# Optimization experiments

Hardware: AMD Instinct MI355X
Metric: run time of the kernel (lower is better)

Reference implementation:

```python
import jax, jax.numpy as jnp
import numpy as np
from jax.ops import segment_sum

N_NODES = 50000
N_EDGES = 800000
D_IN, D_HID, D_OUT = 128, 128, 64


def setup_inputs() -> dict:
    key = jax.random.key(0)
    ks = jax.random.split(key, 7)
    return {
        "src": jax.random.randint(ks[0], (N_EDGES,), 0, N_NODES, dtype=jnp.int32),
        "dst": jax.random.randint(ks[1], (N_EDGES,), 0, N_NODES, dtype=jnp.int32),
        "x": jax.random.normal(ks[2], (N_NODES, D_IN), dtype=jnp.float32),
        "W1": jax.random.normal(ks[3], (D_IN, D_HID), dtype=jnp.float32) * (1.0 / np.sqrt(D_IN)),
        "b1": jnp.zeros((D_HID,), dtype=jnp.float32),
        "W2": jax.random.normal(ks[4], (D_HID, D_OUT), dtype=jnp.float32) * (1.0 / np.sqrt(D_HID)),
        "b2": jnp.zeros((D_OUT,), dtype=jnp.float32),
    }


def _gcn_layer(src, dst, x, W, b, inv_sqrt_out, inv_sqrt_in):
    # DGL GraphConv, norm='both': h = D_in^{-1/2} A D_out^{-1/2} (x W) + b
    h = (x * inv_sqrt_out[:, None]) @ W          # transform first (in >= out)
    msg = h[src]                                  # gather source messages [E, d]
    agg = segment_sum(msg, dst, num_segments=x.shape[0])
    return agg * inv_sqrt_in[:, None] + b


def reference(src, dst, x, W1, b1, W2, b2):
    n = x.shape[0]
    ones = jnp.ones((src.shape[0],), dtype=x.dtype)
    deg_out = jnp.clip(segment_sum(ones, src, num_segments=n), 1.0)
    deg_in = jnp.clip(segment_sum(ones, dst, num_segments=n), 1.0)
    inv_sqrt_out = jax.lax.rsqrt(deg_out)
    inv_sqrt_in = jax.lax.rsqrt(deg_in)
    h = _gcn_layer(src, dst, x, W1, b1, inv_sqrt_out, inv_sqrt_in)
    h = jax.nn.relu(h)
    h = _gcn_layer(src, dst, h, W2, b2, inv_sqrt_out, inv_sqrt_in)
    return h
```

## Files before the change

### kernel.cpp

```cpp
#include <hip/hip_runtime.h>
#include <hip/hip_fp16.h>

#define D_IN  128
#define D_HID 128
#define D_OUT 64
#define NBMAX 512
#define CHUNK 2048
#define FCACHE 3072

typedef __attribute__((ext_vector_type(8))) short bf16x8;
typedef __attribute__((ext_vector_type(4))) float f32x4;

__device__ __forceinline__ unsigned short f2bf_rne(float f) {
    unsigned int u = __float_as_uint(f);
    return (unsigned short)((u + 0x7FFFu + ((u >> 16) & 1u)) >> 16);
}

__launch_bounds__(256)
__global__ void k_prep(const float* __restrict__ W1, const float* __restrict__ W2,
                       unsigned short* __restrict__ W1h, unsigned short* __restrict__ W1l,
                       unsigned short* __restrict__ W2h, unsigned short* __restrict__ W2l,
                       int* __restrict__ cntD, int* __restrict__ cntS, int NB) {
    const int b = blockIdx.x, t = threadIdx.x;
    if (b < 64) {
        const int i = b * 256 + t;
        const int k = i >> 7, j = i & 127;
        const float v = W1[i];
        const unsigned short hb = f2bf_rne(v);
        const float hf = __uint_as_float((unsigned int)hb << 16);
        W1h[j * 128 + k] = hb;
        W1l[j * 128 + k] = f2bf_rne(v - hf);
    } else if (b < 96) {
        const int i = (b - 64) * 256 + t;
        const int k = i >> 6, j = i & 63;
        const float v = W2[i];
        const unsigned short hb = f2bf_rne(v);
        const float hf = __uint_as_float((unsigned int)hb << 16);
        W2h[j * 128 + k] = hb;
        W2l[j * 128 + k] = f2bf_rne(v - hf);
    } else {
        for (int i = t; i < NB; i += 256) { cntD[i] = 0; cntS[i] = 0; }
    }
}

__launch_bounds__(256)
__global__ void k_bucket(const int* __restrict__ src, const int* __restrict__ dst,
                         int E, int NB, int cap,
                         int* __restrict__ cntD, int* __restrict__ cntS,
                         unsigned int* __restrict__ storeD, unsigned char* __restrict__ storeS) {
    __shared__ int lc[512], ls[512];
    __shared__ int baD[512], baS[512];
    __shared__ int gbD[512], gbS[512];
    __shared__ int ssum[256];
    __shared__ unsigned int  ldsD[CHUNK];
    __shared__ int           gposD[CHUNK];
    __shared__ unsigned char ldsS[CHUNK];
    __shared__ int           gposS[CHUNK];

    const int t = threadIdx.x;
    const int e0 = blockIdx.x * CHUNK;
    const int e1 = min(e0 + CHUNK, E);
    const int n  = e1 - e0;

    int sv[8], dv[8];
#pragma unroll
    for (int u = 0; u < 8; ++u) {
        const int i = e0 + u * 256 + t;
        if (i < e1) { sv[u] = src[i]; dv[u] = dst[i]; }
        else        { sv[u] = -1;     dv[u] = -1; }
    }

    lc[t] = 0; lc[t + 256] = 0; ls[t] = 0; ls[t + 256] = 0;
    __syncthreads();
#pragma unroll
    for (int u = 0; u < 8; ++u) {
        if (sv[u] >= 0) {
            atomicAdd(&lc[dv[u] >> 7], 1);
            atomicAdd(&ls[sv[u] >> 7], 1);
        }
    }
    __syncthreads();

    const int c0 = lc[2 * t], c1 = lc[2 * t + 1];
    const int s0 = ls[2 * t], s1 = ls[2 * t + 1];
    {
        const int pc = c0 + c1;
        ssum[t] = pc; __syncthreads();
        int inc = pc;
        for (int off = 1; off < 256; off <<= 1) {
            const int o = (t >= off) ? ssum[t - off] : 0;
            __syncthreads();
            inc += o; ssum[t] = inc;
            __syncthreads();
        }
        const int ex = inc - pc;
        baD[2 * t] = ex; baD[2 * t + 1] = ex + c0;
    }
    {
        const int ps = s0 + s1;
        ssum[t] = ps; __syncthreads();
        int inc = ps;
        for (int off = 1; off < 256; off <<= 1) {
            const int o = (t >= off) ? ssum[t - off] : 0;
            __syncthreads();
            inc += o; ssum[t] = inc;
            __syncthreads();
        }
        const int ex = inc - ps;
        baS[2 * t] = ex; baS[2 * t + 1] = ex + s0;
    }
    __syncthreads();

    for (int i = t; i < NB; i += 256) {
        const int c = lc[i];
        gbD[i] = i * cap + (c ? atomicAdd(&cntD[i], c) : 0);
        const int s = ls[i];
        gbS[i] = i * cap + (s ? atomicAdd(&cntS[i], s) : 0);
    }
    __syncthreads();
    lc[t] = 0; lc[t + 256] = 0; ls[t] = 0; ls[t + 256] = 0;
    __syncthreads();

#pragma unroll
    for (int u = 0; u < 8; ++u) {
        if (sv[u] >= 0) {
            const int s = sv[u], d = dv[u];
            const int bd = d >> 7;
            const int lp = atomicAdd(&lc[bd], 1);
            const int p  = baD[bd] + lp;
            ldsD[p]  = (unsigned int)s | ((unsigned int)(d & 127) << 16);
            gposD[p] = gbD[bd] + lp;
            const int bs = s >> 7;
            const int lq = atomicAdd(&ls[bs], 1);
            const int q  = baS[bs] + lq;
            ldsS[q]  = (unsigned char)(s & 127);
            gposS[q] = gbS[bs] + lq;
        }
    }
    __syncthreads();

    for (int p = t; p < n; p += 256) {
        storeD[gposD[p]] = ldsD[p];
        storeS[gposS[p]] = ldsS[p];
    }
}

__launch_bounds__(256)
__global__ void k_fin(const unsigned int* __restrict__ storeD, const unsigned char* __restrict__ storeS,
                      const int* __restrict__ cntD, const int* __restrict__ cntS,
                      int cap, int N, int NB, int E,
                      int* __restrict__ rowptr, float* __restrict__ inv_in,
                      float* __restrict__ inv_out, unsigned short* __restrict__ csr_src) {
    __shared__ int fh[128];
    __shared__ int sc[128];
    __shared__ int cur[128];
    __shared__ int red[256];
    __shared__ unsigned int ecache[FCACHE];
    const int b = blockIdx.x, t = threadIdx.x;
    const long long sb = (long long)b * cap;

    int partial = 0;
    for (int i = t; i < b; i += 256) partial += cntD[i];
    red[t] = partial;
    __syncthreads();
    for (int off = 128; off > 0; off >>= 1) {
        if (t < off) red[t] += red[t + off];
        __syncthreads();
    }
    const int base = red[0];

    const int cnt = cntD[b];
    const bool cached = (cnt <= FCACHE);
    if (cached) {
        for (int i = t; i < cnt; i += 256) ecache[i] = storeD[sb + i];
    }

    if (t < 128) fh[t] = 0;
    __syncthreads();
    for (int i = t; i < cnt; i += 256) {
        const unsigned int e = cached ? ecache[i] : storeD[sb + i];
        atomicAdd(&fh[e >> 16], 1);
    }
    __syncthreads();
    if (t < 128) sc[t] = fh[t];
    __syncthreads();
    int inc = (t < 128) ? sc[t] : 0;
    for (int off = 1; off < 128; off <<= 1) {
        int o = (t >= off && t < 128) ? sc[t - off] : 0;
        __syncthreads();
        if (t < 128) { inc += o; sc[t] = inc; }
        __syncthreads();
    }
    if (t < 128) {
        const int excl = inc - fh[t];
        cur[t] = excl;
        const int node = (b << 7) + t;
        if (node < N) {
            rowptr[node] = base + excl;
            inv_in[node] = rsqrtf((float)max(fh[t], 1));
        }
    }
    if (b == NB - 1 && t == 128) rowptr[N] = E;
    __syncthreads();
    for (int i = t; i < cnt; i += 256) {
        const unsigned int e = cached ? ecache[i] : storeD[sb + i];
        const int pos = atomicAdd(&cur[e >> 16], 1);
        csr_src[base + pos] = (unsigned short)(e & 0xFFFFu);
    }

    __syncthreads();
    if (t < 128) fh[t] = 0;
    __syncthreads();
    const int cnts = cntS[b];
    for (int i = t; i < cnts; i += 256) atomicAdd(&fh[storeS[sb + i]], 1);
    __syncthreads();
    if (t < 128) {
        const int node = (b << 7) + t;
        if (node < N) inv_out[node] = rsqrtf((float)max(fh[t], 1));
    }
}

template<int LDN, typename TA>
__launch_bounds__(256)
__global__ void k_gemm_mfma(const TA* __restrict__ X,
                            const unsigned short* __restrict__ Wth,
                            const unsigned short* __restrict__ Wtl,
                            const float* __restrict__ scale, __half* __restrict__ Y, int N) {
    __shared__ short Ah[32][136], Al[32][136];

    const int t = threadIdx.x;
    const int row0 = blockIdx.x * 32;

    if constexpr (sizeof(TA) == 4) {
#pragma unroll
        for (int p = 0; p < 4; ++p) {
            const int idx = p * 256 + t;
            const int r   = idx >> 5;
            const int c4  = (idx & 31) << 2;
            const int gr  = row0 + r;
            float4 v = make_float4(0.f, 0.f, 0.f, 0.f);
            if (gr < N) {
                v = *(const float4*)((const float*)X + (long long)gr * 128 + c4);
                if (scale) { const float s = scale[gr]; v.x *= s; v.y *= s; v.z *= s; v.w *= s; }
            }
            const float f[4] = {v.x, v.y, v.z, v.w};
            short hh[4], ll[4];
#pragma unroll
            for (int i = 0; i < 4; ++i) {
                const unsigned short hb = f2bf_rne(f[i]);
                const float hf = __uint_as_float(((unsigned int)hb) << 16);
                hh[i] = (short)hb;
                ll[i] = (short)f2bf_rne(f[i] - hf);
            }
            *(short4*)&Ah[r][c4] = make_short4(hh[0], hh[1], hh[2], hh[3]);
            *(short4*)&Al[r][c4] = make_short4(ll[0], ll[1], ll[2], ll[3]);
        }
    } else {
#pragma unroll
        for (int p = 0; p < 2; ++p) {
            const int idx = p * 256 + t;
            const int r   = idx >> 4;
            const int c8  = (idx & 15) << 3;
            const int gr  = row0 + r;
            uint4 raw = make_uint4(0u, 0u, 0u, 0u);
            if (gr < N) raw = *(const uint4*)((const __half*)X + (long long)gr * 128 + c8);
            const __half2* hp = (const __half2*)&raw;
            short hh[8], ll[8];
#pragma unroll
            for (int u = 0; u < 4; ++u) {
                const float2 f2 = __half22float2(hp[u]);
                const float f[2] = {f2.x, f2.y};
#pragma unroll
                for (int q = 0; q < 2; ++q) {
                    const unsigned short hb = f2bf_rne(f[q]);
                    const float hf = __uint_as_float(((unsigned int)hb) << 16);
                    hh[2 * u + q] = (short)hb;
                    ll[2 * u + q] = (short)f2bf_rne(f[q] - hf);
                }
            }
            *(short4*)&Ah[r][c8]     = make_short4(hh[0], hh[1], hh[2], hh[3]);
            *(short4*)&Ah[r][c8 + 4] = make_short4(hh[4], hh[5], hh[6], hh[7]);
            *(short4*)&Al[r][c8]     = make_short4(ll[0], ll[1], ll[2], ll[3]);
            *(short4*)&Al[r][c8 + 4] = make_short4(ll[4], ll[5], ll[6], ll[7]);
        }
    }
    __syncthreads();

    constexpr int NT = LDN / 32;
    const int w    = t >> 6;
    const int lane = t & 63;
    const int rg = w & 1, cg = w >> 1;
    const int lrow = lane & 15;
    const int lk   = (lane >> 4) << 3;
    const int colbase = cg * (16 * NT);

    f32x4 acc[NT];
#pragma unroll
    for (int n = 0; n < NT; ++n) acc[n] = (f32x4){0.f, 0.f, 0.f, 0.f};

#pragma unroll
    for (int ks = 0; ks < 4; ++ks) {
        const int k = ks * 32 + lk;
        const bf16x8 ah = *(const bf16x8*)&Ah[rg * 16 + lrow][k];
        const bf16x8 al = *(const bf16x8*)&Al[rg * 16 + lrow][k];
#pragma unroll
        for (int n = 0; n < NT; ++n) {
            const int col = colbase + n * 16 + lrow;
            const bf16x8 bh = *(const bf16x8*)(Wth + (size_t)col * 128 + k);
            const bf16x8 bl = *(const bf16x8*)(Wtl + (size_t)col * 128 + k);
            acc[n] = __builtin_amdgcn_mfma_f32_16x16x32_bf16(ah, bh, acc[n], 0, 0, 0);
            acc[n] = __builtin_amdgcn_mfma_f32_16x16x32_bf16(ah, bl, acc[n], 0, 0, 0);
            acc[n] = __builtin_amdgcn_mfma_f32_16x16x32_bf16(al, bh, acc[n], 0, 0, 0);
        }
    }

#pragma unroll
    for (int n = 0; n < NT; ++n) {
#pragma unroll
        for (int i = 0; i < 4; ++i) {
            const int r = row0 + rg * 16 + ((lane >> 4) << 2) + i;
            if (r < N)
                Y[(long long)r * LDN + colbase + n * 16 + lrow] = __float2half(acc[n][i]);
        }
    }
}

template<int D, bool RELU, typename TO>
__launch_bounds__(256)
__global__ void k_gather(const int* __restrict__ rowptr, const unsigned short* __restrict__ csr_src,
                         const __half* __restrict__ Y, const float* __restrict__ inv_in,
                         const float* __restrict__ inv_out, const float* __restrict__ b,
                         TO* __restrict__ out, int N) {
    const int wid  = (int)((blockIdx.x * 256u + threadIdx.x) >> 6);
    const int lane = threadIdx.x & 63;
    if (wid >= N) return;

    const int start = rowptr[wid];
    const int end   = rowptr[wid + 1];

    constexpr int LPE = D / 8;
    constexpr int EPW = 64 / LPE;
    const int grp  = lane / LPE;
    const int colh = (lane % LPE) * 8;

    float a[8];
#pragma unroll
    for (int u = 0; u < 8; ++u) a[u] = 0.0f;

    auto accum = [&](uint4 raw) {
        const __half2* h = (const __half2*)&raw;
#pragma unroll
        for (int u = 0; u < 4; ++u) {
            const float2 f = __half22float2(h[u]);
            a[2 * u]     += f.x;
            a[2 * u + 1] += f.y;
        }
    };

    for (int k = start; k < end; k += 64) {
        const int idx = k + lane;
        const int sv  = (idx < end) ? (int)csr_src[idx] : 0;
        const int cnt = min(64, end - k);
        int j = 0;
        for (; j + 8 * EPW <= cnt; j += 8 * EPW) {
            int s[8];
#pragma unroll
            for (int u = 0; u < 8; ++u) s[u] = __shfl(sv, j + u * EPW + grp);
            uint4 r[8];
#pragma unroll
            for (int u = 0; u < 8; ++u) r[u] = *(const uint4*)(Y + (long long)s[u] * D + colh);
#pragma unroll
            for (int u = 0; u < 8; ++u) accum(r[u]);
        }
        for (; j + 4 * EPW <= cnt; j += 4 * EPW) {
            int s[4];
#pragma unroll
            for (int u = 0; u < 4; ++u) s[u] = __shfl(sv, j + u * EPW + grp);
            uint4 r[4];
#pragma unroll
            for (int u = 0; u < 4; ++u) r[u] = *(const uint4*)(Y + (long long)s[u] * D + colh);
#pragma unroll
            for (int u = 0; u < 4; ++u) accum(r[u]);
        }
        for (; j < cnt; j += EPW) {
            const int jj = j + grp;
            const int s  = __shfl(sv, jj);
            if (jj < cnt) {
                const uint4 r = *(const uint4*)(Y + (long long)s * D + colh);
                accum(r);
            }
        }
    }

#pragma unroll
    for (int u = 0; u < 8; ++u) a[u] += __shfl_down(a[u], 32);
#pragma unroll
    for (int u = 0; u < 8; ++u) a[u] += __shfl_down(a[u], 16);
    if (EPW == 8) {
#pragma unroll
        for (int u = 0; u < 8; ++u) a[u] += __shfl_down(a[u], 8);
    }

    if (lane < LPE) {
        const float ii = inv_in[wid];
        const float io = RELU ? inv_out[wid] : 0.0f;
        const float4 b0 = *(const float4*)(b + colh);
        const float4 b1 = *(const float4*)(b + colh + 4);
        float r[8];
        r[0] = a[0] * ii + b0.x; r[1] = a[1] * ii + b0.y;
        r[2] = a[2] * ii + b0.z; r[3] = a[3] * ii + b0.w;
        r[4] = a[4] * ii + b1.x; r[5] = a[5] * ii + b1.y;
        r[6] = a[6] * ii + b1.z; r[7] = a[7] * ii + b1.w;
        if (RELU) {
#pragma unroll
            for (int u = 0; u < 8; ++u) r[u] = fmaxf(r[u], 0.0f) * io;
        }
        if constexpr (sizeof(TO) == 2) {
            __half2 h0 = __float22half2_rn(make_float2(r[0], r[1]));
            __half2 h1 = __float22half2_rn(make_float2(r[2], r[3]));
            __half2 h2 = __float22half2_rn(make_float2(r[4], r[5]));
            __half2 h3 = __float22half2_rn(make_float2(r[6], r[7]));
            uint4 pk;
            pk.x = *(unsigned int*)&h0; pk.y = *(unsigned int*)&h1;
            pk.z = *(unsigned int*)&h2; pk.w = *(unsigned int*)&h3;
            *(uint4*)((__half*)out + (long long)wid * D + colh) = pk;
        } else {
            float* o = (float*)out + (long long)wid * D + colh;
            *(float4*)(o)     = make_float4(r[0], r[1], r[2], r[3]);
            *(float4*)(o + 4) = make_float4(r[4], r[5], r[6], r[7]);
        }
    }
}

extern "C" void kernel_launch(void* const* d_in, const int* in_sizes, int n_in,
                              void* d_out, int out_size, void* d_ws, size_t ws_size,
                              hipStream_t stream) {
    const int*   src = (const int*)d_in[0];
    const int*   dst = (const int*)d_in[1];
    const float* x   = (const float*)d_in[2];
    const float* W1  = (const float*)d_in[3];
    const float* b1  = (const float*)d_in[4];
    const float* W2  = (const float*)d_in[5];
    const float* b2  = (const float*)d_in[6];
    float* out = (float*)d_out;

    const int E  = in_sizes[0];
    const int N  = in_sizes[2] / D_IN;
    const int NB = (N + 127) >> 7;
    const int mean = E / NB;
    const int cap  = mean + mean / 4 + 128;

    char* ws = (char*)d_ws;
    size_t off = 0;
    auto alloc = [&](size_t bytes) -> void* {
        void* p = ws + off;
        off += (bytes + 255) & ~(size_t)255;
        return p;
    };
    float*          inv_out = (float*)alloc((size_t)N * 4);
    float*          inv_in  = (float*)alloc((size_t)N * 4);
    int*            rowptr  = (int*)alloc((size_t)(N + 1) * 4);
    int*            cntD    = (int*)alloc((size_t)NB * 4);
    int*            cntS    = (int*)alloc((size_t)NB * 4);
    unsigned int*   storeD  = (unsigned int*)alloc((size_t)NB * cap * 4);
    unsigned char*  storeS  = (unsigned char*)alloc((size_t)NB * cap);
    unsigned short* csr_src = (unsigned short*)alloc((size_t)E * 2);
    unsigned short* W1h     = (unsigned short*)alloc(128 * 128 * 2);
    unsigned short* W1l     = (unsigned short*)alloc(128 * 128 * 2);
    unsigned short* W2h     = (unsigned short*)alloc(64 * 128 * 2);
    unsigned short* W2l     = (unsigned short*)alloc(64 * 128 * 2);
    __half*         Y1      = (__half*)alloc((size_t)N * D_HID * 2);
    __half*         H       = (__half*)alloc((size_t)N * D_HID * 2);
    __half*         Y2      = (__half*)alloc((size_t)N * D_OUT * 2);
    (void)ws_size; (void)n_in; (void)out_size;

    k_prep<<<97, 256, 0, stream>>>(W1, W2, W1h, W1l, W2h, W2l, cntD, cntS, NB);
    k_bucket<<<(E + CHUNK - 1) / CHUNK, 256, 0, stream>>>(src, dst, E, NB, cap, cntD, cntS, storeD, storeS);
    k_fin<<<NB, 256, 0, stream>>>(storeD, storeS, cntD, cntS, cap, N, NB, E,
                                  rowptr, inv_in, inv_out, csr_src);

    k_gemm_mfma<D_HID, float><<<(N + 31) / 32, 256, 0, stream>>>(x, W1h, W1l, inv_out, Y1, N);
    k_gather<D_HID, true, __half><<<(N + 3) / 4, 256, 0, stream>>>(rowptr, csr_src, Y1, inv_in, inv_out, b1, H, N);

    k_gemm_mfma<D_OUT, __half><<<(N + 31) / 32, 256, 0, stream>>>(H, W2h, W2l, nullptr, Y2, N);
    k_gather<D_OUT, false, float><<<(N + 3) / 4, 256, 0, stream>>>(rowptr, csr_src, Y2, inv_in, nullptr, b2, out, N);
}
```

Baseline: 140.9 us.

## Overlap first-layer GEMM with edge bucketing by moving source scaling into gather

The out-degree scaling of x is moved from the first GEMM into the first gather, where each gathered source row is multiplied by inv_out[src]. The first GEMM no longer depends on the degree computation, so it is merged into the bucketing kernel as extra blocks that share LDS through a union. This lets the GEMM run concurrently with the scatter-heavy bucketing and removes one launch. In exchange, the gather does an extra scalar load per edge, and the merged kernel's LDS footprint is sized by the larger bucket layout, which may lower occupancy for the GEMM blocks.

```diff
diff --git a/kernel.cpp b/kernel.cpp
--- a/kernel.cpp
+++ b/kernel.cpp
@@ -43,22 +43,30 @@
     }
 }
 
-__launch_bounds__(256)
-__global__ void k_bucket(const int* __restrict__ src, const int* __restrict__ dst,
-                         int E, int NB, int cap,
-                         int* __restrict__ cntD, int* __restrict__ cntS,
-                         unsigned int* __restrict__ storeD, unsigned char* __restrict__ storeS) {
-    __shared__ int lc[512], ls[512];
-    __shared__ int baD[512], baS[512];
-    __shared__ int gbD[512], gbS[512];
-    __shared__ int ssum[256];
-    __shared__ unsigned int  ldsD[CHUNK];
-    __shared__ int           gposD[CHUNK];
-    __shared__ unsigned char ldsS[CHUNK];
-    __shared__ int           gposS[CHUNK];
-
+struct BucketS {
+    int lc[512], ls[512];
+    int baD[512], baS[512];
+    int gbD[512], gbS[512];
+    int ssum[256];
+    unsigned int  ldsD[CHUNK];
+    int           gposD[CHUNK];
+    unsigned char ldsS[CHUNK];
+    int           gposS[CHUNK];
+};
+struct GemmS {
+    short Ah[32][136];
+    short Al[32][136];
+};
+union SMem { BucketS b; GemmS g; };
+
+__device__ __forceinline__ void bucket_body(
+        BucketS& sm, int bx,
+        const int* __restrict__ src, const int* __restrict__ dst,
+        int E, int NB, int cap,
+        int* __restrict__ cntD, int* __restrict__ cntS,
+        unsigned int* __restrict__ storeD, unsigned char* __restrict__ storeS) {
     const int t = threadIdx.x;
-    const int e0 = blockIdx.x * CHUNK;
+    const int e0 = bx * CHUNK;
     const int e1 = min(e0 + CHUNK, E);
     const int n  = e1 - e0;
 
@@ -70,55 +78,55 @@
         else        { sv[u] = -1;     dv[u] = -1; }
     }
 
-    lc[t] = 0; lc[t + 256] = 0; ls[t] = 0; ls[t + 256] = 0;
+    sm.lc[t] = 0; sm.lc[t + 256] = 0; sm.ls[t] = 0; sm.ls[t + 256] = 0;
     __syncthreads();
 #pragma unroll
     for (int u = 0; u < 8; ++u) {
         if (sv[u] >= 0) {
-            atomicAdd(&lc[dv[u] >> 7], 1);
-            atomicAdd(&ls[sv[u] >> 7], 1);
-        }
-    }
-    __syncthreads();
-
-    const int c0 = lc[2 * t], c1 = lc[2 * t + 1];
-    const int s0 = ls[2 * t], s1 = ls[2 * t + 1];
+            atomicAdd(&sm.lc[dv[u] >> 7], 1);
+            atomicAdd(&sm.ls[sv[u] >> 7], 1);
+        }
+    }
+    __syncthreads();
+
+    const int c0 = sm.lc[2 * t], c1 = sm.lc[2 * t + 1];
+    const int s0 = sm.ls[2 * t], s1 = sm.ls[2 * t + 1];
     {
         const int pc = c0 + c1;
-        ssum[t] = pc; __syncthreads();
+        sm.ssum[t] = pc; __syncthreads();
         int inc = pc;
         for (int off = 1; off < 256; off <<= 1) {
-            const int o = (t >= off) ? ssum[t - off] : 0;
+            const int o = (t >= off) ? sm.ssum[t - off] : 0;
             __syncthreads();
-            inc += o; ssum[t] = inc;
+            inc += o; sm.ssum[t] = inc;
             __syncthreads();
         }
         const int ex = inc - pc;
-        baD[2 * t] = ex; baD[2 * t + 1] = ex + c0;
+        sm.baD[2 * t] = ex; sm.baD[2 * t + 1] = ex + c0;
     }
     {
         const int ps = s0 + s1;
-        ssum[t] = ps; __syncthreads();
+        sm.ssum[t] = ps; __syncthreads();
         int inc = ps;
         for (int off = 1; off < 256; off <<= 1) {
-            const int o = (t >= off) ? ssum[t - off] : 0;
+            const int o = (t >= off) ? sm.ssum[t - off] : 0;
             __syncthreads();
-            inc += o; ssum[t] = inc;
+            inc += o; sm.ssum[t] = inc;
             __syncthreads();
         }
         const int ex = inc - ps;
-        baS[2 * t] = ex; baS[2 * t + 1] = ex + s0;
+        sm.baS[2 * t] = ex; sm.baS[2 * t + 1] = ex + s0;
     }
     __syncthreads();
 
     for (int i = t; i < NB; i += 256) {
-        const int c = lc[i];
-        gbD[i] = i * cap + (c ? atomicAdd(&cntD[i], c) : 0);
-        const int s = ls[i];
-        gbS[i] = i * cap + (s ? atomicAdd(&cntS[i], s) : 0);
-    }
-    __syncthreads();
-    lc[t] = 0; lc[t + 256] = 0; ls[t] = 0; ls[t + 256] = 0;
+        const int c = sm.lc[i];
+        sm.gbD[i] = i * cap + (c ? atomicAdd(&cntD[i], c) : 0);
+        const int s = sm.ls[i];
+        sm.gbS[i] = i * cap + (s ? atomicAdd(&cntS[i], s) : 0);
+    }
+    __syncthreads();
+    sm.lc[t] = 0; sm.lc[t + 256] = 0; sm.ls[t] = 0; sm.ls[t + 256] = 0;
     __syncthreads();
 
 #pragma unroll
@@ -126,23 +134,109 @@
         if (sv[u] >= 0) {
             const int s = sv[u], d = dv[u];
             const int bd = d >> 7;
-            const int lp = atomicAdd(&lc[bd], 1);
-            const int p  = baD[bd] + lp;
-            ldsD[p]  = (unsigned int)s | ((unsigned int)(d & 127) << 16);
-            gposD[p] = gbD[bd] + lp;
+            const int lp = atomicAdd(&sm.lc[bd], 1);
+            const int p  = sm.baD[bd] + lp;
+            sm.ldsD[p]  = (unsigned int)s | ((unsigned int)(d & 127) << 16);
+            sm.gposD[p] = sm.gbD[bd] + lp;
             const int bs = s >> 7;
-            const int lq = atomicAdd(&ls[bs], 1);
-            const int q  = baS[bs] + lq;
-            ldsS[q]  = (unsigned char)(s & 127);
-            gposS[q] = gbS[bs] + lq;
+            const int lq = atomicAdd(&sm.ls[bs], 1);
+            const int q  = sm.baS[bs] + lq;
+            sm.ldsS[q]  = (unsigned char)(s & 127);
+            sm.gposS[q] = sm.gbS[bs] + lq;
         }
     }
     __syncthreads();
 
     for (int p = t; p < n; p += 256) {
-        storeD[gposD[p]] = ldsD[p];
-        storeS[gposS[p]] = ldsS[p];
-    }
+        storeD[sm.gposD[p]] = sm.ldsD[p];
+        storeS[sm.gposS[p]] = sm.ldsS[p];
+    }
+}
+
+__device__ __forceinline__ void gemm1_body(
+        GemmS& sm, int bx,
+        const float* __restrict__ X,
+        const unsigned short* __restrict__ Wth, const unsigned short* __restrict__ Wtl,
+        __half* __restrict__ Y, int N) {
+    const int t = threadIdx.x;
+    const int row0 = bx * 32;
+
+#pragma unroll
+    for (int p = 0; p < 4; ++p) {
+        const int idx = p * 256 + t;
+        const int r   = idx >> 5;
+        const int c4  = (idx & 31) << 2;
+        const int gr  = row0 + r;
+        float4 v = make_float4(0.f, 0.f, 0.f, 0.f);
+        if (gr < N) v = *(const float4*)(X + (long long)gr * 128 + c4);
+        const float f[4] = {v.x, v.y, v.z, v.w};
+        short hh[4], ll[4];
+#pragma unroll
+        for (int i = 0; i < 4; ++i) {
+            const unsigned short hb = f2bf_rne(f[i]);
+            const float hf = __uint_as_float(((unsigned int)hb) << 16);
+            hh[i] = (short)hb;
+            ll[i] = (short)f2bf_rne(f[i] - hf);
+        }
+        *(short4*)&sm.Ah[r][c4] = make_short4(hh[0], hh[1], hh[2], hh[3]);
+        *(short4*)&sm.Al[r][c4] = make_short4(ll[0], ll[1], ll[2], ll[3]);
+    }
+    __syncthreads();
+
+    constexpr int NT = 4;
+    const int w    = t >> 6;
+    const int lane = t & 63;
+    const int rg = w & 1, cg = w >> 1;
+    const int lrow = lane & 15;
+    const int lk   = (lane >> 4) << 3;
+    const int colbase = cg * (16 * NT);
+
+    f32x4 acc[NT];
+#pragma unroll
+    for (int n = 0; n < NT; ++n) acc[n] = (f32x4){0.f, 0.f, 0.f, 0.f};
+
+#pragma unroll
+    for (int ks = 0; ks < 4; ++ks) {
+        const int k = ks * 32 + lk;
+        const bf16x8 ah = *(const bf16x8*)&sm.Ah[rg * 16 + lrow][k];
+        const bf16x8 al = *(const bf16x8*)&sm.Al[rg * 16 + lrow][k];
+#pragma unroll
+        for (int n = 0; n < NT; ++n) {
+            const int col = colbase + n * 16 + lrow;
+            const bf16x8 bh = *(const bf16x8*)(Wth + (size_t)col * 128 + k);
+            const bf16x8 bl = *(const bf16x8*)(Wtl + (size_t)col * 128 + k);
+            acc[n] = __builtin_amdgcn_mfma_f32_16x16x32_bf16(ah, bh, acc[n], 0, 0, 0);
+            acc[n] = __builtin_amdgcn_mfma_f32_16x16x32_bf16(ah, bl, acc[n], 0, 0, 0);
+            acc[n] = __builtin_amdgcn_mfma_f32_16x16x32_bf16(al, bh, acc[n], 0, 0, 0);
+        }
+    }
+
+#pragma unroll
+    for (int n = 0; n < NT; ++n) {
+#pragma unroll
+        for (int i = 0; i < 4; ++i) {
+            const int r = row0 + rg * 16 + ((lane >> 4) << 2) + i;
+            if (r < N)
+                Y[(long long)r * D_HID + colbase + n * 16 + lrow] = __float2half(acc[n][i]);
+        }
+    }
+}
+
+__launch_bounds__(256)
+__global__ void k_bucket_gemm(const int* __restrict__ src, const int* __restrict__ dst,
+                              int E, int NB, int cap,
+                              int* __restrict__ cntD, int* __restrict__ cntS,
+                              unsigned int* __restrict__ storeD, unsigned char* __restrict__ storeS,
+                              const float* __restrict__ X,
+                              const unsigned short* __restrict__ Wth,
+                              const unsigned short* __restrict__ Wtl,
+                              __half* __restrict__ Y, int N, int nbBlk) {
+    __shared__ SMem sm;
+    const int bx = (int)blockIdx.x;
+    if (bx < nbBlk)
+        bucket_body(sm.b, bx, src, dst, E, NB, cap, cntD, cntS, storeD, storeS);
+    else
+        gemm1_body(sm.g, bx - nbBlk, X, Wth, Wtl, Y, N);
 }
 
 __launch_bounds__(256)
@@ -220,69 +314,43 @@
     }
 }
 
-template<int LDN, typename TA>
+template<int LDN>
 __launch_bounds__(256)
-__global__ void k_gemm_mfma(const TA* __restrict__ X,
+__global__ void k_gemm_mfma(const __half* __restrict__ X,
                             const unsigned short* __restrict__ Wth,
                             const unsigned short* __restrict__ Wtl,
-                            const float* __restrict__ scale, __half* __restrict__ Y, int N) {
+                            __half* __restrict__ Y, int N) {
     __shared__ short Ah[32][136], Al[32][136];
 
     const int t = threadIdx.x;
     const int row0 = blockIdx.x * 32;
 
-    if constexpr (sizeof(TA) == 4) {
-#pragma unroll
-        for (int p = 0; p < 4; ++p) {
-            const int idx = p * 256 + t;
-            const int r   = idx >> 5;
-            const int c4  = (idx & 31) << 2;
-            const int gr  = row0 + r;
-            float4 v = make_float4(0.f, 0.f, 0.f, 0.f);
-            if (gr < N) {
-                v = *(const float4*)((const float*)X + (long long)gr * 128 + c4);
-                if (scale) { const float s = scale[gr]; v.x *= s; v.y *= s; v.z *= s; v.w *= s; }
+#pragma unroll
+    for (int p = 0; p < 2; ++p) {
+        const int idx = p * 256 + t;
+        const int r   = idx >> 4;
+        const int c8  = (idx & 15) << 3;
+        const int gr  = row0 + r;
+        uint4 raw = make_uint4(0u, 0u, 0u, 0u);
+        if (gr < N) raw = *(const uint4*)(X + (long long)gr * 128 + c8);
+        const __half2* hp = (const __half2*)&raw;
+        short hh[8], ll[8];
+#pragma unroll
+        for (int u = 0; u < 4; ++u) {
+            const float2 f2 = __half22float2(hp[u]);
+            const float f[2] = {f2.x, f2.y};
+#pragma unroll
+            for (int q = 0; q < 2; ++q) {
+                const unsigned short hb = f2bf_rne(f[q]);
+                const float hf = __uint_as_float(((unsigned int)hb) << 16);
+                hh[2 * u + q] = (short)hb;
+                ll[2 * u + q] = (short)f2bf_rne(f[q] - hf);
             }
-            const float f[4] = {v.x, v.y, v.z, v.w};
-            short hh[4], ll[4];
-#pragma unroll
-            for (int i = 0; i < 4; ++i) {
-                const unsigned short hb = f2bf_rne(f[i]);
-                const float hf = __uint_as_float(((unsigned int)hb) << 16);
-                hh[i] = (short)hb;
-                ll[i] = (short)f2bf_rne(f[i] - hf);
-            }
-            *(short4*)&Ah[r][c4] = make_short4(hh[0], hh[1], hh[2], hh[3]);
-            *(short4*)&Al[r][c4] = make_short4(ll[0], ll[1], ll[2], ll[3]);
-        }
-    } else {
-#pragma unroll
-        for (int p = 0; p < 2; ++p) {
-            const int idx = p * 256 + t;
-            const int r   = idx >> 4;
-            const int c8  = (idx & 15) << 3;
-            const int gr  = row0 + r;
-            uint4 raw = make_uint4(0u, 0u, 0u, 0u);
-            if (gr < N) raw = *(const uint4*)((const __half*)X + (long long)gr * 128 + c8);
-            const __half2* hp = (const __half2*)&raw;
-            short hh[8], ll[8];
-#pragma unroll
-            for (int u = 0; u < 4; ++u) {
-                const float2 f2 = __half22float2(hp[u]);
-                const float f[2] = {f2.x, f2.y};
-#pragma unroll
-                for (int q = 0; q < 2; ++q) {
-                    const unsigned short hb = f2bf_rne(f[q]);
-                    const float hf = __uint_as_float(((unsigned int)hb) << 16);
-                    hh[2 * u + q] = (short)hb;
-                    ll[2 * u + q] = (short)f2bf_rne(f[q] - hf);
-                }
-            }
-            *(short4*)&Ah[r][c8]     = make_short4(hh[0], hh[1], hh[2], hh[3]);
-            *(short4*)&Ah[r][c8 + 4] = make_short4(hh[4], hh[5], hh[6], hh[7]);
-            *(short4*)&Al[r][c8]     = make_short4(ll[0], ll[1], ll[2], ll[3]);
-            *(short4*)&Al[r][c8 + 4] = make_short4(ll[4], ll[5], ll[6], ll[7]);
-        }
+        }
+        *(short4*)&Ah[r][c8]     = make_short4(hh[0], hh[1], hh[2], hh[3]);
+        *(short4*)&Ah[r][c8 + 4] = make_short4(hh[4], hh[5], hh[6], hh[7]);
+        *(short4*)&Al[r][c8]     = make_short4(ll[0], ll[1], ll[2], ll[3]);
+        *(short4*)&Al[r][c8 + 4] = make_short4(ll[4], ll[5], ll[6], ll[7]);
     }
     __syncthreads();
 
@@ -325,12 +393,12 @@
     }
 }
 
-template<int D, bool RELU, typename TO>
+template<int D, bool RELU, bool SRCSCALE, typename TO>
 __launch_bounds__(256)
 __global__ void k_gather(const int* __restrict__ rowptr, const unsigned short* __restrict__ csr_src,
                          const __half* __restrict__ Y, const float* __restrict__ inv_in,
                          const float* __restrict__ inv_out, const float* __restrict__ b,
-                         TO* __restrict__ out, int N) {
+                         TO* __restrict__ out, int N, const float* __restrict__ inv_src) {
     const int wid  = (int)((blockIdx.x * 256u + threadIdx.x) >> 6);
     const int lane = threadIdx.x & 63;
     if (wid >= N) return;
@@ -347,13 +415,18 @@
 #pragma unroll
     for (int u = 0; u < 8; ++u) a[u] = 0.0f;
 
-    auto accum = [&](uint4 raw) {
+    auto accum = [&](uint4 raw, float io) {
         const __half2* h = (const __half2*)&raw;
 #pragma unroll
         for (int u = 0; u < 4; ++u) {
             const float2 f = __half22float2(h[u]);
-            a[2 * u]     += f.x;
-            a[2 * u + 1] += f.y;
+            if constexpr (SRCSCALE) {
+                a[2 * u]     += f.x * io;
+                a[2 * u + 1] += f.y * io;
+            } else {
+                a[2 * u]     += f.x;
+                a[2 * u + 1] += f.y;
+            }
         }
     };
 
@@ -369,8 +442,13 @@
             uint4 r[8];
 #pragma unroll
             for (int u = 0; u < 8; ++u) r[u] = *(const uint4*)(Y + (long long)s[u] * D + colh);
-#pragma unroll
-            for (int u = 0; u < 8; ++u) accum(r[u]);
+            float io[8];
+            if constexpr (SRCSCALE) {
+#pragma unroll
+                for (int u = 0; u < 8; ++u) io[u] = inv_src[s[u]];
+            }
+#pragma unroll
+            for (int u = 0; u < 8; ++u) accum(r[u], SRCSCALE ? io[u] : 0.0f);
         }
         for (; j + 4 * EPW <= cnt; j += 4 * EPW) {
             int s[4];
@@ -379,15 +457,20 @@
             uint4 r[4];
 #pragma unroll
             for (int u = 0; u < 4; ++u) r[u] = *(const uint4*)(Y + (long long)s[u] * D + colh);
-#pragma unroll
-            for (int u = 0; u < 4; ++u) accum(r[u]);
+            float io[4];
+            if constexpr (SRCSCALE) {
+#pragma unroll
+                for (int u = 0; u < 4; ++u) io[u] = inv_src[s[u]];
+            }
+#pragma unroll
+            for (int u = 0; u < 4; ++u) accum(r[u], SRCSCALE ? io[u] : 0.0f);
         }
         for (; j < cnt; j += EPW) {
             const int jj = j + grp;
             const int s  = __shfl(sv, jj);
             if (jj < cnt) {
                 const uint4 r = *(const uint4*)(Y + (long long)s * D + colh);
-                accum(r);
+                accum(r, SRCSCALE ? inv_src[s] : 0.0f);
             }
         }
     }
@@ -474,14 +557,19 @@
     __half*         Y2      = (__half*)alloc((size_t)N * D_OUT * 2);
     (void)ws_size; (void)n_in; (void)out_size;
 
+    const int nbBlk   = (E + CHUNK - 1) / CHUNK;
+    const int gemmBlk = (N + 31) / 32;
+
     k_prep<<<97, 256, 0, stream>>>(W1, W2, W1h, W1l, W2h, W2l, cntD, cntS, NB);
-    k_bucket<<<(E + CHUNK - 1) / CHUNK, 256, 0, stream>>>(src, dst, E, NB, cap, cntD, cntS, storeD, storeS);
+    k_bucket_gemm<<<nbBlk + gemmBlk, 256, 0, stream>>>(src, dst, E, NB, cap, cntD, cntS,
+                                                       storeD, storeS, x, W1h, W1l, Y1, N, nbBlk);
     k_fin<<<NB, 256, 0, stream>>>(storeD, storeS, cntD, cntS, cap, N, NB, E,
                                   rowptr, inv_in, inv_out, csr_src);
 
-    k_gemm_mfma<D_HID, float><<<(N + 31) / 32, 256, 0, stream>>>(x, W1h, W1l, inv_out, Y1, N);
-    k_gather<D_HID, true, __half><<<(N + 3) / 4, 256, 0, stream>>>(rowptr, csr_src, Y1, inv_in, inv_out, b1, H, N);
-
-    k_gemm_mfma<D_OUT, __half><<<(N + 31) / 32, 256, 0, stream>>>(H, W2h, W2l, nullptr, Y2, N);
-    k_gather<D_OUT, false, float><<<(N + 3) / 4, 256, 0, stream>>>(rowptr, csr_src, Y2, inv_in, nullptr, b2, out, N);
-}
+    k_gather<D_HID, true, true, __half><<<(N + 3) / 4, 256, 0, stream>>>(
+        rowptr, csr_src, Y1, inv_in, inv_out, b1, H, N, inv_out);
+
+    k_gemm_mfma<D_OUT><<<(N + 31) / 32, 256, 0, stream>>>(H, W2h, W2l, Y2, N);
+    k_gather<D_OUT, false, false, float><<<(N + 3) / 4, 256, 0, stream>>>(
+        rowptr, csr_src, Y2, inv_in, nullptr, b2, out, N, nullptr);
+}
```

Measured after the change: 134.1 us. 1.05x faster.
